# Performance work log

Measured on AMD Instinct MI355X. Metric: run time of the kernel, lower is better.

## Reference

```python
import jax, jax.numpy as jnp
import numpy as np

SEQLEN, BATCH, FEAT = 512, 64, 512
HID, WIN, LAYERS, OUT, NSPK = 1024, 16, 3, 512, 2


def setup_inputs() -> dict:
    key = jax.random.key(0)
    ks = jax.random.split(key, 16)
    s = 0.05  # small init scale to keep activations stable
    return {
        "h": jax.random.normal(ks[0], (SEQLEN, BATCH, FEAT), jnp.float32),
        "Wa": jax.random.normal(ks[1], (NSPK, HID, FEAT), jnp.float32) * s,
        "Wih0": jax.random.normal(ks[2], (4 * HID, FEAT), jnp.float32) * s,
        "Whh0": jax.random.normal(ks[3], (4 * HID, HID), jnp.float32) * s,
        "bih0": jax.random.normal(ks[4], (4 * HID,), jnp.float32) * s,
        "bhh0": jax.random.normal(ks[5], (4 * HID,), jnp.float32) * s,
        "Wih_rest": jax.random.normal(ks[6], (LAYERS - 1, 4 * HID, HID), jnp.float32) * s,
        "Whh_rest": jax.random.normal(ks[7], (LAYERS - 1, 4 * HID, HID), jnp.float32) * s,
        "bih_rest": jax.random.normal(ks[8], (LAYERS - 1, 4 * HID), jnp.float32) * s,
        "bhh_rest": jax.random.normal(ks[9], (LAYERS - 1, 4 * HID), jnp.float32) * s,
        "Wfc": jax.random.normal(ks[10], (OUT, HID + FEAT), jnp.float32) * s,
        "bfc": jax.random.normal(ks[11], (OUT,), jnp.float32) * s,
        "s0": jax.random.normal(ks[12], (BATCH, HID), jnp.float32),
        "h0": jax.random.normal(ks[13], (LAYERS, BATCH, HID), jnp.float32),
        "c0": jax.random.normal(ks[14], (LAYERS, BATCH, HID), jnp.float32),
    }


def _lstm_cell(x, h_prev, c_prev, Wih, Whh, bih, bhh):
    # torch.nn.LSTMCell math; only the new h is consumed downstream
    g = x @ Wih.T + bih + h_prev @ Whh.T + bhh  # [B, 4H]
    i, f, gg, o = jnp.split(g, 4, axis=1)
    c_new = jax.nn.sigmoid(f) * c_prev + jax.nn.sigmoid(i) * jnp.tanh(gg)
    return jax.nn.sigmoid(o) * jnp.tanh(c_new)


def reference(h, Wa, Wih0, Whh0, bih0, bhh0, Wih_rest, Whh_rest, bih_rest, bhh_rest, Wfc, bfc, s0, h0, c0):
    T, B, F = h.shape
    win_len = 2 * WIN + 1
    pad = jnp.zeros((WIN, B, F), h.dtype)
    h_pad = jnp.concatenate([pad, h, pad], axis=0)  # [T+2W, B, F]

    def make_step(Wa_s):
        def step(s_prev, i):
            window = jax.lax.dynamic_slice(h_pad, (i, 0, 0), (win_len, B, F))  # [w,B,F]
            proj = s_prev @ Wa_s                       # [B,F]
            e = jnp.einsum('bf,wbf->wb', proj, window)  # attention energies
            a = jax.nn.softmax(e, axis=0)
            c_t = jnp.einsum('wb,wbf->bf', a, window)   # context [B,F]
            x = _lstm_cell(c_t, h0[0], c0[0], Wih0, Whh0, bih0, bhh0)
            for l in range(Wih_rest.shape[0]):  # fixed small layer count
                x = _lstm_cell(x, h0[l + 1], c0[l + 1], Wih_rest[l], Whh_rest[l], bih_rest[l], bhh_rest[l])
            out = jax.nn.relu(jnp.concatenate([x, c_t], axis=1) @ Wfc.T + bfc)
            return x, out  # s_before for next step carries across speakers too
        return step

    outs = []
    s = s0
    for sp in range(Wa.shape[0]):
        s, o = jax.lax.scan(make_step(Wa[sp]), s, jnp.arange(T))
        outs.append(o)
    return jnp.stack(outs)  # [num_speaker, T, B, OUT]
```

## Files before the change

kernel.cpp:

```cpp
#include <hip/hip_runtime.h>

#define T_LEN 512
#define BATCH 64
#define FEATD 512
#define HID   1024
#define G4H   4096
#define WINR  16
#define WLEN  33
#define OUTD  512
#define CATD  1536
#define NBLK  256
#define NTHR  512

typedef unsigned int uint32;
typedef unsigned long long u64;
typedef unsigned short ushort16;
typedef short s16x8 __attribute__((ext_vector_type(8)));
typedef float f32x4 __attribute__((ext_vector_type(4)));

static const size_t OFF_U    = 0;
static const size_t OFF_HH   = 33554432;
static const size_t OFF_S    = OFF_HH + 786432;
static const size_t OFF_CB   = OFF_S  + 65536;
static const size_t OFF_X1   = OFF_CB + 16384;
static const size_t OFF_X2   = OFF_X1 + 32768;
static const size_t OFF_CK   = OFF_X2 + 32768;
static const size_t OFF_XK   = OFF_CK + 262144;
static const size_t OFF_BAR  = OFF_XK + 524288;
static const size_t OFF_WFCB = OFF_BAR + 1024;

__device__ __forceinline__ float sigmoidf_(float x) { return 1.0f / (1.0f + expf(-x)); }
__device__ __forceinline__ ushort16 f2bf(float f) {
  uint32 u = __float_as_uint(f);
  uint32 r = u + 0x7FFFu + ((u >> 16) & 1u);
  return (ushort16)(r >> 16);
}

__device__ __forceinline__ uint2 aload8(const void* p) {
  u64 v = __hip_atomic_load((const u64*)p, __ATOMIC_RELAXED, __HIP_MEMORY_SCOPE_AGENT);
  uint2 r; r.x = (unsigned)(v & 0xffffffffull); r.y = (unsigned)(v >> 32);
  return r;
}
__device__ __forceinline__ float aload4f(const void* p) {
  return __hip_atomic_load((const float*)p, __ATOMIC_RELAXED, __HIP_MEMORY_SCOPE_AGENT);
}
__device__ __forceinline__ void astore8(void* p, u64 v) {
  __hip_atomic_store((u64*)p, v, __ATOMIC_RELAXED, __HIP_MEMORY_SCOPE_AGENT);
}
__device__ __forceinline__ void astore4f(void* p, float v) {
  __hip_atomic_store((float*)p, v, __ATOMIC_RELAXED, __HIP_MEMORY_SCOPE_AGENT);
}

__device__ __forceinline__ void grid_barrier(unsigned* bar) {
  __syncthreads();
  if (threadIdx.x == 0) {
    unsigned* cnt  = bar + ((blockIdx.x & 7u) << 6);
    unsigned* gcnt = bar + 512;
    unsigned* gen  = bar + 576;
    unsigned g = __hip_atomic_load(gen, __ATOMIC_RELAXED, __HIP_MEMORY_SCOPE_AGENT);
    unsigned a = __hip_atomic_fetch_add(cnt, 1u, __ATOMIC_RELAXED, __HIP_MEMORY_SCOPE_AGENT);
    if (a == 31u) {
      __hip_atomic_store(cnt, 0u, __ATOMIC_RELAXED, __HIP_MEMORY_SCOPE_AGENT);
      unsigned ga = __hip_atomic_fetch_add(gcnt, 1u, __ATOMIC_RELAXED, __HIP_MEMORY_SCOPE_AGENT);
      if (ga == 7u) {
        __hip_atomic_store(gcnt, 0u, __ATOMIC_RELAXED, __HIP_MEMORY_SCOPE_AGENT);
        __hip_atomic_fetch_add(gen, 1u, __ATOMIC_RELAXED, __HIP_MEMORY_SCOPE_AGENT);
      } else {
        while (__hip_atomic_load(gen, __ATOMIC_RELAXED, __HIP_MEMORY_SCOPE_AGENT) == g)
          __builtin_amdgcn_s_sleep(2);
      }
    } else {
      while (__hip_atomic_load(gen, __ATOMIC_RELAXED, __HIP_MEMORY_SCOPE_AGENT) == g)
        __builtin_amdgcn_s_sleep(2);
    }
  }
  __syncthreads();
}

template<int KSTEPS>
__device__ __forceinline__ void lstm_stage_mfma(
    const ushort16* __restrict__ wl,
    const ushort16* __restrict__ actB4,
    const float* __restrict__ hhg,
    float c0v,
    ushort16* __restrict__ xoutB4,
    ushort16* __restrict__ xhist_slot,
    float* __restrict__ sOut,
    float* __restrict__ red,
    float* __restrict__ hv_l)
{
  const int tid  = threadIdx.x;
  const int wv   = tid >> 6;
  const int lane = tid & 63;
  const int nt   = wv & 3;
  const int kh   = wv >> 2;
  const int quad = lane >> 4;
  const int b    = nt * 16 + (lane & 15);
  const int half = KSTEPS / 2;

  f32x4 acc0 = {0.f, 0.f, 0.f, 0.f};
  f32x4 acc1 = {0.f, 0.f, 0.f, 0.f};
  #pragma unroll
  for (int i = 0; i < half; i += 2) {
    const int ks0 = kh * half + i;
    const int ks1 = ks0 + 1;
    s16x8 a0 = *(const s16x8*)(wl + ((size_t)ks0 * 64 + lane) * 8);
    s16x8 a1 = *(const s16x8*)(wl + ((size_t)ks1 * 64 + lane) * 8);
    const int g0 = ks0 * 8 + quad * 2;
    const int g1 = ks1 * 8 + quad * 2;
    uint2 lo0 = aload8(actB4 + ((size_t)g0 * 64 + b) * 4);
    uint2 hi0 = aload8(actB4 + ((size_t)(g0 + 1) * 64 + b) * 4);
    uint2 lo1 = aload8(actB4 + ((size_t)g1 * 64 + b) * 4);
    uint2 hi1 = aload8(actB4 + ((size_t)(g1 + 1) * 64 + b) * 4);
    union { uint4 u; s16x8 v; } b0, b1;
    b0.u = make_uint4(lo0.x, lo0.y, hi0.x, hi0.y);
    b1.u = make_uint4(lo1.x, lo1.y, hi1.x, hi1.y);
    acc0 = __builtin_amdgcn_mfma_f32_16x16x32_bf16(a0, b0.v, acc0, 0, 0, 0);
    acc1 = __builtin_amdgcn_mfma_f32_16x16x32_bf16(a1, b1.v, acc1, 0, 0, 0);
  }
  f32x4 acc = acc0 + acc1;
  {
    float* rp = red + (((size_t)(kh * 4 + nt) * 16 + quad * 4) * 16) + (lane & 15);
    rp[0]  = acc[0];
    rp[16] = acc[1];
    rp[32] = acc[2];
    rp[48] = acc[3];
  }
  __syncthreads();
  if (wv < 4) {
    const int jl = wv;
    const int bb = lane;
    const int ntb = bb >> 4, col = bb & 15;
    float g[4];
    #pragma unroll
    for (int gate = 0; gate < 4; ++gate) {
      const int m = gate * 4 + jl;
      g[gate] = red[((size_t)(0 + ntb) * 16 + m) * 16 + col]
              + red[((size_t)(4 + ntb) * 16 + m) * 16 + col]
              + hhg[gate];
    }
    float cn = sigmoidf_(g[1]) * c0v + sigmoidf_(g[0]) * tanhf(g[2]);
    float hv = sigmoidf_(g[3]) * tanhf(cn);
    if (sOut) astore4f(sOut + (size_t)bb * HID + (blockIdx.x << 2) + jl, hv);
    hv_l[jl * 64 + bb] = hv;
  }
  if (xoutB4 || xhist_slot) {
    __syncthreads();
    if (wv == 0) {
      const int bb = lane;
      uint32 lo = (uint32)f2bf(hv_l[0 * 64 + bb]) | ((uint32)f2bf(hv_l[1 * 64 + bb]) << 16);
      uint32 hi = (uint32)f2bf(hv_l[2 * 64 + bb]) | ((uint32)f2bf(hv_l[3 * 64 + bb]) << 16);
      u64 pk = ((u64)hi << 32) | (u64)lo;
      if (xoutB4)     astore8(xoutB4 + ((size_t)blockIdx.x * 64 + bb) * 4, pk);
      if (xhist_slot) astore8(xhist_slot + ((size_t)blockIdx.x * 64 + bb) * 4, pk);
    }
  }
}

__device__ __forceinline__ void fc_step_mfma(int tp, int sub,
    const ushort16* __restrict__ ch4,
    const ushort16* __restrict__ xh4,
    const ushort16* __restrict__ Wfcb,
    const float* __restrict__ bfc,
    float* __restrict__ outp, float* __restrict__ red)
{
  const int tid  = threadIdx.x;
  const int wv   = tid >> 6;
  const int lane = tid & 63;
  const int slot = tp & 15;
  const int ot   = sub >> 1;
  const int tsel = wv & 1;
  const int kq   = wv >> 1;
  const int quad = lane >> 4;
  const int b    = ((sub & 1) * 2 + tsel) * 16 + (lane & 15);
  const ushort16* xs = xh4 + (size_t)slot * 65536;
  const ushort16* cs = ch4 + (size_t)slot * 32768;
  const ushort16* wa = Wfcb + ((size_t)ot * 48 + (size_t)kq * 12) * 512;

  f32x4 acc0 = {0.f, 0.f, 0.f, 0.f};
  f32x4 acc1 = {0.f, 0.f, 0.f, 0.f};
  #pragma unroll
  for (int i = 0; i < 12; i += 2) {
    const int ks0 = kq * 12 + i;
    const int ks1 = ks0 + 1;
    s16x8 a0 = *(const s16x8*)(wa + (size_t)i * 512 + (size_t)lane * 8);
    s16x8 a1 = *(const s16x8*)(wa + (size_t)(i + 1) * 512 + (size_t)lane * 8);
    const ushort16* s0p = (ks0 < 32) ? xs : cs;
    const ushort16* s1p = (ks1 < 32) ? xs : cs;
    const int gg0 = ((ks0 < 32) ? ks0 * 8 : (ks0 - 32) * 8) + quad * 2;
    const int gg1 = ((ks1 < 32) ? ks1 * 8 : (ks1 - 32) * 8) + quad * 2;
    uint2 lo0 = aload8(s0p + ((size_t)gg0 * 64 + b) * 4);
    uint2 hi0 = aload8(s0p + ((size_t)(gg0 + 1) * 64 + b) * 4);
    uint2 lo1 = aload8(s1p + ((size_t)gg1 * 64 + b) * 4);
    uint2 hi1 = aload8(s1p + ((size_t)(gg1 + 1) * 64 + b) * 4);
    union { uint4 u; s16x8 v; } b0, b1;
    b0.u = make_uint4(lo0.x, lo0.y, hi0.x, hi0.y);
    b1.u = make_uint4(lo1.x, lo1.y, hi1.x, hi1.y);
    acc0 = __builtin_amdgcn_mfma_f32_16x16x32_bf16(a0, b0.v, acc0, 0, 0, 0);
    acc1 = __builtin_amdgcn_mfma_f32_16x16x32_bf16(a1, b1.v, acc1, 0, 0, 0);
  }
  f32x4 acc = acc0 + acc1;
  {
    float* rp = red + ((size_t)wv * 16 + quad * 4) * 16 + (lane & 15);
    rp[0]  = acc[0];
    rp[16] = acc[1];
    rp[32] = acc[2];
    rp[48] = acc[3];
  }
  __syncthreads();
  {
    const int tl   = tid >> 8;
    const int bcol = (tid >> 4) & 15;
    const int m    = tid & 15;
    float v = bfc[ot * 16 + m];
    #pragma unroll
    for (int k4 = 0; k4 < 4; ++k4)
      v += red[((size_t)(k4 * 2 + tl) * 16 + m) * 16 + bcol];
    const int bo = ((sub & 1) * 2 + tl) * 16 + bcol;
    outp[((size_t)tp * BATCH + bo) * OUTD + ot * 16 + m] = fmaxf(v, 0.f);
  }
}

__global__ void __launch_bounds__(NTHR)
decoder_kernel(const float* __restrict__ hin, const float* __restrict__ u,
               const float* __restrict__ Wih0, const float* __restrict__ Wihr,
               const ushort16* __restrict__ Wfcb, const float* __restrict__ bfc,
               const float* __restrict__ c0, const float* __restrict__ hhT,
               float* __restrict__ s,
               ushort16* __restrict__ x1B4, ushort16* __restrict__ x2B4,
               ushort16* __restrict__ chist4, ushort16* __restrict__ xhist4,
               unsigned* __restrict__ bar, float* __restrict__ outp)
{
  __shared__ ushort16 wlds[40960];
  __shared__ float s_l[HID];
  __shared__ float e_l[64];
  __shared__ float a_l[64];
  __shared__ float red[2 * 4 * 16 * 16];
  __shared__ float c_l[FEATD];
  __shared__ float hv_l[4 * 64];

  const int tid  = threadIdx.x;
  const int bid  = blockIdx.x;
  const int wv   = tid >> 6;
  const int lane = tid & 63;

  for (int r = tid; r < 40960; r += NTHR) {
    int local, ksz; const float* Wsrc;
    if (r < 8192)        { local = r;         ksz = FEATD; Wsrc = Wih0; }
    else if (r < 24576)  { local = r - 8192;  ksz = HID;   Wsrc = Wihr; }
    else                 { local = r - 24576; ksz = HID;   Wsrc = Wihr + (size_t)G4H * HID; }
    const int ks   = local >> 9;
    const int li   = local & 511;
    const int ln   = li >> 3;
    const int jj   = li & 7;
    const int m    = ln & 15;
    const int quad = ln >> 4;
    const int k    = ks * 32 + quad * 8 + jj;
    const int n    = (m >> 2) * HID + (bid << 2) + (m & 3);
    wlds[r] = f2bf(Wsrc[(size_t)n * ksz + k]);
  }

  float hh_r[3][4];
  float c0_r[3];
  if (wv < 4) {
    const int j  = (bid << 2) + wv;
    const int bb = lane;
    #pragma unroll
    for (int l = 0; l < 3; ++l) {
      #pragma unroll
      for (int gate = 0; gate < 4; ++gate)
        hh_r[l][gate] = hhT[((size_t)l * G4H + (size_t)gate * HID + j) * 64 + bb];
      c0_r[l] = c0[((size_t)l * BATCH + bb) * HID + j];
    }
  } else {
    #pragma unroll
    for (int l = 0; l < 3; ++l) {
      hh_r[l][0] = hh_r[l][1] = hh_r[l][2] = hh_r[l][3] = 0.f;
      c0_r[l] = 0.f;
    }
  }
  __syncthreads();

  for (int t = 0; t < T_LEN; ++t) {
    const int slot = t & 15;
    if (bid < BATCH) {
      const int b = bid;
      s_l[tid]        = aload4f(s + (size_t)b * HID + tid);
      s_l[tid + NTHR] = aload4f(s + (size_t)b * HID + tid + NTHR);
      __syncthreads();
      for (int w = wv; w < WLEN; w += 8) {
        const int tau = t + w - WINR;
        float e = 0.f;
        if (tau >= 0 && tau < T_LEN) {
          const float* up = u + ((size_t)tau * BATCH + b) * HID;
          #pragma unroll
          for (int i = 0; i < 16; ++i) {
            const int hidx = lane + (i << 6);
            e += s_l[hidx] * up[hidx];
          }
          #pragma unroll
          for (int m = 32; m; m >>= 1) e += __shfl_xor(e, m);
        }
        if (lane == 0) e_l[w] = e;
      }
      __syncthreads();
      if (tid < 64) {
        float e = (tid < WLEN) ? e_l[tid] : -1e30f;
        float mx = e;
        #pragma unroll
        for (int m = 32; m; m >>= 1) mx = fmaxf(mx, __shfl_xor(mx, m));
        float p = (tid < WLEN) ? expf(e - mx) : 0.f;
        float sm = p;
        #pragma unroll
        for (int m = 32; m; m >>= 1) sm += __shfl_xor(sm, m);
        if (tid < WLEN) a_l[tid] = p / sm;
      }
      __syncthreads();
      {
        const int w0 = (t < WINR) ? (WINR - t) : 0;
        const int w1 = (T_LEN + WINR - t < WLEN) ? (T_LEN + WINR - t) : WLEN;
        const size_t hstep = (size_t)BATCH * FEATD;
        const float* hp = hin + ((size_t)(t + w0 - WINR) * BATCH + b) * FEATD + tid;
        float ca = 0.f, cb = 0.f;
        int w = w0;
        for (; w + 1 < w1; w += 2) {
          ca = fmaf(a_l[w],     hp[0],     ca);
          cb = fmaf(a_l[w + 1], hp[hstep], cb);
          hp += 2 * hstep;
        }
        if (w < w1) ca = fmaf(a_l[w], hp[0], ca);
        c_l[tid] = ca + cb;
      }
      __syncthreads();
      if (tid < 128) {
        uint32 lo = (uint32)f2bf(c_l[4 * tid + 0]) | ((uint32)f2bf(c_l[4 * tid + 1]) << 16);
        uint32 hi = (uint32)f2bf(c_l[4 * tid + 2]) | ((uint32)f2bf(c_l[4 * tid + 3]) << 16);
        u64 pk = ((u64)hi << 32) | (u64)lo;
        astore8(chist4 + (size_t)slot * 32768 + ((size_t)tid * 64 + b) * 4, pk);
      }
    } else if (t >= 3 && t % 3 == 0) {
      const int fb = bid - BATCH;
      const int tp = t - 3 + (fb >> 6);
      fc_step_mfma(tp, fb & 63, chist4, xhist4, Wfcb, bfc, outp, red);
    }
    grid_barrier(bar);
    lstm_stage_mfma<16>(wlds, chist4 + (size_t)slot * 32768, hh_r[0], c0_r[0],
                        x1B4, nullptr, nullptr, red, hv_l);
    grid_barrier(bar);
    lstm_stage_mfma<32>(wlds + 8192, x1B4, hh_r[1], c0_r[1],
                        x2B4, nullptr, nullptr, red, hv_l);
    grid_barrier(bar);
    lstm_stage_mfma<32>(wlds + 24576, x2B4, hh_r[2], c0_r[2],
                        nullptr, xhist4 + (size_t)slot * 65536, s, red, hv_l);
    grid_barrier(bar);
  }
  if (bid < 128) {
    const int tp = 510 + (bid >> 6);
    fc_step_mfma(tp, bid & 63, chist4, xhist4, Wfcb, bfc, outp, red);
  }
}

__global__ void __launch_bounds__(256)
wfcswz_kernel(const float* __restrict__ Wfc, ushort16* __restrict__ Wfcb)
{
  const int idx = blockIdx.x * 256 + threadIdx.x;
  const int ot  = idx / 24576;
  const int r   = idx - ot * 24576;
  const int ks  = r >> 9;
  const int li  = r & 511;
  const int ln  = li >> 3;
  const int j   = li & 7;
  const int k   = ks * 32 + (ln >> 4) * 8 + j;
  const int o   = ot * 16 + (ln & 15);
  Wfcb[idx] = f2bf(Wfc[(size_t)o * CATD + k]);
}

__global__ void __launch_bounds__(256)
gemm_u_kernel(const float* __restrict__ A, const float* __restrict__ Bm,
              float* __restrict__ C)
{
  __shared__ float Al[64 * 68];
  __shared__ float Bl[64 * 68];
  const int tid = threadIdx.x;
  const int m0 = blockIdx.x * 64;
  const int n0 = blockIdx.y * 64;
  const int tx = tid & 15, ty = tid >> 4;
  float acc[4][4] = {};
  for (int kc = 0; kc < 512; kc += 64) {
    #pragma unroll
    for (int p = 0; p < 4; ++p) {
      const int row = p * 16 + (tid >> 4);
      const int kq  = (tid & 15) * 4;
      float4 v = *(const float4*)(A + (size_t)(m0 + row) * 512 + kc + kq);
      Al[(kq + 0) * 68 + row] = v.x;
      Al[(kq + 1) * 68 + row] = v.y;
      Al[(kq + 2) * 68 + row] = v.z;
      Al[(kq + 3) * 68 + row] = v.w;
      float4 w = *(const float4*)(Bm + (size_t)(n0 + row) * 512 + kc + kq);
      Bl[(kq + 0) * 68 + row] = w.x;
      Bl[(kq + 1) * 68 + row] = w.y;
      Bl[(kq + 2) * 68 + row] = w.z;
      Bl[(kq + 3) * 68 + row] = w.w;
    }
    __syncthreads();
    #pragma unroll 8
    for (int k = 0; k < 64; ++k) {
      float4 av = *(const float4*)(&Al[k * 68 + ty * 4]);
      float4 bv = *(const float4*)(&Bl[k * 68 + tx * 4]);
      float aa[4] = {av.x, av.y, av.z, av.w};
      float bb[4] = {bv.x, bv.y, bv.z, bv.w};
      #pragma unroll
      for (int i = 0; i < 4; ++i)
        #pragma unroll
        for (int jj = 0; jj < 4; ++jj)
          acc[i][jj] = fmaf(aa[i], bb[jj], acc[i][jj]);
    }
    __syncthreads();
  }
  #pragma unroll
  for (int i = 0; i < 4; ++i) {
    float4 r = {acc[i][0], acc[i][1], acc[i][2], acc[i][3]};
    *(float4*)(C + (size_t)(m0 + ty * 4 + i) * 1024 + n0 + tx * 4) = r;
  }
}

__global__ void __launch_bounds__(256)
hhconst_kernel(const float* __restrict__ Whh0, const float* __restrict__ Whr,
               const float* __restrict__ bih0, const float* __restrict__ bhh0,
               const float* __restrict__ bihr, const float* __restrict__ bhhr,
               const float* __restrict__ h0, float* __restrict__ hh)
{
  const int idx = blockIdx.x * 256 + threadIdx.x;
  const int b = idx & 63;
  const int n = (idx >> 6) & 4095;
  const int l = idx >> 18;
  const float* W = (l == 0) ? (Whh0 + (size_t)n * HID)
                            : (Whr + ((size_t)(l - 1) * G4H + n) * HID);
  float acc = ((l == 0) ? bih0[n] : bihr[(l - 1) * G4H + n])
            + ((l == 0) ? bhh0[n] : bhhr[(l - 1) * G4H + n]);
  const float* hr = h0 + ((size_t)l * BATCH + b) * HID;
  #pragma unroll 2
  for (int k = 0; k < HID; k += 4) {
    float4 a4 = *(const float4*)(hr + k);
    float4 w4 = *(const float4*)(W + k);
    acc += a4.x * w4.x + a4.y * w4.y + a4.z * w4.z + a4.w * w4.w;
  }
  hh[idx] = acc;
}

__global__ void __launch_bounds__(256)
init_kernel(const float* __restrict__ s0, float* __restrict__ s, unsigned* __restrict__ bar)
{
  const int gid = blockIdx.x * 256 + threadIdx.x;
  if (gid < BATCH * HID) s[gid] = s0[gid];
  if (blockIdx.x == 0)
    for (int i = threadIdx.x; i < 1024; i += 256) bar[i] = 0u;
}

extern "C" void kernel_launch(void* const* d_in, const int* in_sizes, int n_in,
                              void* d_out, int out_size, void* d_ws, size_t ws_size,
                              hipStream_t stream) {
  (void)in_sizes; (void)n_in; (void)out_size; (void)ws_size;
  const float* h    = (const float*)d_in[0];
  const float* Wa   = (const float*)d_in[1];
  const float* Wih0 = (const float*)d_in[2];
  const float* Whh0 = (const float*)d_in[3];
  const float* bih0 = (const float*)d_in[4];
  const float* bhh0 = (const float*)d_in[5];
  const float* Wihr = (const float*)d_in[6];
  const float* Whhr = (const float*)d_in[7];
  const float* bihr = (const float*)d_in[8];
  const float* bhhr = (const float*)d_in[9];
  const float* Wfc  = (const float*)d_in[10];
  const float* bfc  = (const float*)d_in[11];
  const float* s0   = (const float*)d_in[12];
  const float* h0   = (const float*)d_in[13];
  const float* c0   = (const float*)d_in[14];
  float* out = (float*)d_out;
  float* ws  = (float*)d_ws;

  float* u         = ws + OFF_U;
  float* hhT       = ws + OFF_HH;
  float* s         = ws + OFF_S;
  ushort16* x1B4   = (ushort16*)(ws + OFF_X1);
  ushort16* x2B4   = (ushort16*)(ws + OFF_X2);
  ushort16* chist4 = (ushort16*)(ws + OFF_CK);
  ushort16* xhist4 = (ushort16*)(ws + OFF_XK);
  unsigned* bar    = (unsigned*)(ws + OFF_BAR);
  ushort16* Wfcb   = (ushort16*)(ws + OFF_WFCB);

  hipLaunchKernelGGL(init_kernel, dim3(256), dim3(256), 0, stream, s0, s, bar);
  hipLaunchKernelGGL(hhconst_kernel, dim3(3072), dim3(256), 0, stream,
                     Whh0, Whhr, bih0, bhh0, bihr, bhhr, h0, hhT);
  hipLaunchKernelGGL(wfcswz_kernel, dim3(3072), dim3(256), 0, stream, Wfc, Wfcb);
  for (int sp = 0; sp < 2; ++sp) {
    hipLaunchKernelGGL(gemm_u_kernel, dim3(512, 16), dim3(256), 0, stream,
                       h, Wa + (size_t)sp * HID * FEATD, u);
    hipLaunchKernelGGL(decoder_kernel, dim3(NBLK), dim3(NTHR), 0, stream,
                       h, u, Wih0, Wihr, Wfcb, bfc, c0, hhT, s,
                       x1B4, x2B4, chist4, xhist4, bar,
                       out + (size_t)sp * T_LEN * BATCH * OUTD);
  }
}
```

Baseline: 36.43 ms.

## Use monotonic epoch-based grid barrier, prefetch next window, widen context accumulation

```diff
diff --git a/kernel.cpp b/kernel.cpp
--- a/kernel.cpp
+++ b/kernel.cpp
@@ -51,28 +51,17 @@
   __hip_atomic_store((float*)p, v, __ATOMIC_RELAXED, __HIP_MEMORY_SCOPE_AGENT);
 }
 
-__device__ __forceinline__ void grid_barrier(unsigned* bar) {
+__device__ __forceinline__ void grid_barrier(unsigned* bar, unsigned epoch) {
   __syncthreads();
   if (threadIdx.x == 0) {
     unsigned* cnt  = bar + ((blockIdx.x & 7u) << 6);
-    unsigned* gcnt = bar + 512;
-    unsigned* gen  = bar + 576;
-    unsigned g = __hip_atomic_load(gen, __ATOMIC_RELAXED, __HIP_MEMORY_SCOPE_AGENT);
+    unsigned* gsum = bar + 512;
     unsigned a = __hip_atomic_fetch_add(cnt, 1u, __ATOMIC_RELAXED, __HIP_MEMORY_SCOPE_AGENT);
-    if (a == 31u) {
-      __hip_atomic_store(cnt, 0u, __ATOMIC_RELAXED, __HIP_MEMORY_SCOPE_AGENT);
-      unsigned ga = __hip_atomic_fetch_add(gcnt, 1u, __ATOMIC_RELAXED, __HIP_MEMORY_SCOPE_AGENT);
-      if (ga == 7u) {
-        __hip_atomic_store(gcnt, 0u, __ATOMIC_RELAXED, __HIP_MEMORY_SCOPE_AGENT);
-        __hip_atomic_fetch_add(gen, 1u, __ATOMIC_RELAXED, __HIP_MEMORY_SCOPE_AGENT);
-      } else {
-        while (__hip_atomic_load(gen, __ATOMIC_RELAXED, __HIP_MEMORY_SCOPE_AGENT) == g)
-          __builtin_amdgcn_s_sleep(2);
-      }
-    } else {
-      while (__hip_atomic_load(gen, __ATOMIC_RELAXED, __HIP_MEMORY_SCOPE_AGENT) == g)
-        __builtin_amdgcn_s_sleep(2);
-    }
+    if (((a + 1u) & 31u) == 0u)
+      __hip_atomic_fetch_add(gsum, 1u, __ATOMIC_RELAXED, __HIP_MEMORY_SCOPE_AGENT);
+    const unsigned target = epoch * 8u;
+    while ((int)(__hip_atomic_load(gsum, __ATOMIC_RELAXED, __HIP_MEMORY_SCOPE_AGENT) - target) < 0)
+      __builtin_amdgcn_s_sleep(2);
   }
   __syncthreads();
 }
@@ -281,10 +270,20 @@
   }
   __syncthreads();
 
+  unsigned ep = 0;
   for (int t = 0; t < T_LEN; ++t) {
     const int slot = t & 15;
     if (bid < BATCH) {
       const int b = bid;
+      float pf0 = 0.f, pf1 = 0.f, pf2 = 0.f;
+      {
+        const int taun = t + 1 + WINR;
+        if (taun < T_LEN) {
+          pf0 = u[((size_t)taun * BATCH + b) * HID + tid];
+          pf1 = u[((size_t)taun * BATCH + b) * HID + tid + NTHR];
+          pf2 = hin[((size_t)taun * BATCH + b) * FEATD + tid];
+        }
+      }
       s_l[tid]        = aload4f(s + (size_t)b * HID + tid);
       s_l[tid + NTHR] = aload4f(s + (size_t)b * HID + tid + NTHR);
       __syncthreads();
@@ -321,15 +320,17 @@
         const int w1 = (T_LEN + WINR - t < WLEN) ? (T_LEN + WINR - t) : WLEN;
         const size_t hstep = (size_t)BATCH * FEATD;
         const float* hp = hin + ((size_t)(t + w0 - WINR) * BATCH + b) * FEATD + tid;
-        float ca = 0.f, cb = 0.f;
+        float c0a = 0.f, c1a = 0.f, c2a = 0.f, c3a = 0.f;
         int w = w0;
-        for (; w + 1 < w1; w += 2) {
-          ca = fmaf(a_l[w],     hp[0],     ca);
-          cb = fmaf(a_l[w + 1], hp[hstep], cb);
-          hp += 2 * hstep;
+        for (; w + 3 < w1; w += 4) {
+          c0a = fmaf(a_l[w],     hp[0],         c0a);
+          c1a = fmaf(a_l[w + 1], hp[hstep],     c1a);
+          c2a = fmaf(a_l[w + 2], hp[2 * hstep], c2a);
+          c3a = fmaf(a_l[w + 3], hp[3 * hstep], c3a);
+          hp += 4 * hstep;
         }
-        if (w < w1) ca = fmaf(a_l[w], hp[0], ca);
-        c_l[tid] = ca + cb;
+        for (; w < w1; ++w) { c0a = fmaf(a_l[w], hp[0], c0a); hp += hstep; }
+        c_l[tid] = (c0a + c1a) + (c2a + c3a);
       }
       __syncthreads();
       if (tid < 128) {
@@ -338,26 +339,33 @@
         u64 pk = ((u64)hi << 32) | (u64)lo;
         astore8(chist4 + (size_t)slot * 32768 + ((size_t)tid * 64 + b) * 4, pk);
       }
+      asm volatile("" :: "v"(pf0), "v"(pf1), "v"(pf2));
     } else if (t >= 3 && t % 3 == 0) {
       const int fb = bid - BATCH;
       const int tp = t - 3 + (fb >> 6);
       fc_step_mfma(tp, fb & 63, chist4, xhist4, Wfcb, bfc, outp, red);
     }
-    grid_barrier(bar);
+    grid_barrier(bar, ++ep);
     lstm_stage_mfma<16>(wlds, chist4 + (size_t)slot * 32768, hh_r[0], c0_r[0],
                         x1B4, nullptr, nullptr, red, hv_l);
-    grid_barrier(bar);
+    grid_barrier(bar, ++ep);
     lstm_stage_mfma<32>(wlds + 8192, x1B4, hh_r[1], c0_r[1],
                         x2B4, nullptr, nullptr, red, hv_l);
-    grid_barrier(bar);
+    grid_barrier(bar, ++ep);
     lstm_stage_mfma<32>(wlds + 24576, x2B4, hh_r[2], c0_r[2],
                         nullptr, xhist4 + (size_t)slot * 65536, s, red, hv_l);
-    grid_barrier(bar);
+    grid_barrier(bar, ++ep);
   }
   if (bid < 128) {
     const int tp = 510 + (bid >> 6);
     fc_step_mfma(tp, bid & 63, chist4, xhist4, Wfcb, bfc, outp, red);
   }
+}
+
+__global__ void __launch_bounds__(256)
+barreset_kernel(unsigned* __restrict__ bar)
+{
+  for (int i = threadIdx.x; i < 1024; i += 256) bar[i] = 0u;
 }
 
 __global__ void __launch_bounds__(256)
@@ -496,6 +504,7 @@
   for (int sp = 0; sp < 2; ++sp) {
     hipLaunchKernelGGL(gemm_u_kernel, dim3(512, 16), dim3(256), 0, stream,
                        h, Wa + (size_t)sp * HID * FEATD, u);
+    hipLaunchKernelGGL(barreset_kernel, dim3(1), dim3(256), 0, stream, bar);
     hipLaunchKernelGGL(decoder_kernel, dim3(NBLK), dim3(NTHR), 0, stream,
                        h, u, Wih0, Wihr, Wfcb, bfc, c0, hhT, s,
                        x1B4, x2B4, chist4, xhist4, bar,
```

New measurement: 36.42 ms. No clear change (-0.0%).
